# Performance work log

Measured on AMD Instinct MI355X. Metric: run time of the kernel, lower is better.

The kernel has to match this reference:

```python
import jax, jax.numpy as jnp
import numpy as np

D_MODEL = 1024
NUM_HEADS = 16
NEG_INF = jnp.float32(-(2.0 ** 32) + 1.0)  # matches TF's -2**32+1 padding value


def setup_inputs() -> dict:
    key = jax.random.key(0)
    ks = jax.random.split(key, 10)
    B, S, D = 4, 1024, D_MODEL
    s = 1.0 / np.sqrt(D)
    return {
        "q": jax.random.normal(ks[0], (B, S, D), jnp.float32),
        "k": jax.random.normal(ks[1], (B, S, D), jnp.float32),
        "v": jax.random.normal(ks[2], (B, S, D), jnp.float32),
        "mask": jax.random.randint(ks[3], (NUM_HEADS * B, 1, S), 0, 2, jnp.int32),
        "Wq": jax.random.normal(ks[4], (D, D), jnp.float32) * s,
        "bq": jnp.zeros((D,), jnp.float32),
        "Wk": jax.random.normal(ks[5], (D, D), jnp.float32) * s,
        "bk": jnp.zeros((D,), jnp.float32),
        "Wv": jax.random.normal(ks[6], (D, D), jnp.float32) * s,
        "bv": jnp.zeros((D,), jnp.float32),
    }


def _split_heads(x, h):
    # TF: concat(split(x, h, axis=2), axis=0) -> head index leading on batch dim
    B, S, D = x.shape
    dh = D // h
    return x.reshape(B, S, h, dh).transpose(2, 0, 1, 3).reshape(h * B, S, dh)


def _merge_heads(x, h):
    hB, S, dh = x.shape
    B = hB // h
    return x.reshape(h, B, S, dh).transpose(1, 2, 0, 3).reshape(B, S, h * dh)


def reference(q, k, v, mask, Wq, bq, Wk, bk, Wv, bv):
    h = NUM_HEADS
    qp = q @ Wq + bq
    kp = k @ Wk + bk
    vp = v @ Wv + bv
    qh = _split_heads(qp, h)  # [h*B, S, dh]
    kh = _split_heads(kp, h)
    vh = _split_heads(vp, h)
    dh = kh.shape[-1]
    logits = jnp.einsum('bqd,bkd->bqk', qh, kh) / jnp.sqrt(jnp.float32(dh))
    logits = jnp.where(mask == 0, NEG_INF, logits)  # padding mask, broadcast [h*B,1,S]
    S = qh.shape[1]
    causal = jnp.tril(jnp.ones((S, S), jnp.bool_))
    logits = jnp.where(causal[None], logits, NEG_INF)
    attn = jax.nn.softmax(logits, axis=-1)
    out = jnp.einsum('bqk,bkd->bqd', attn, vh)
    return _merge_heads(out, h)  # [B, S, d_model]
```

## Files before the change

### kernel.cpp

```cpp
#include <hip/hip_runtime.h>
#include <stdint.h>

#define DEV __device__ __forceinline__

typedef __attribute__((ext_vector_type(4))) float f32x4;
typedef __attribute__((ext_vector_type(8))) __bf16 bf16x8;
typedef __attribute__((ext_vector_type(8))) unsigned short ushort8;
typedef __attribute__((ext_vector_type(4))) unsigned short u16x4;
typedef __attribute__((ext_vector_type(4))) int i32x4;
typedef __attribute__((ext_vector_type(2))) unsigned int u32x2;

DEV unsigned short f2bf(float f) {
    union { float f; unsigned int u; } v; v.f = f;
    unsigned int r = v.u + 0x7FFFu + ((v.u >> 16) & 1u);
    return (unsigned short)(r >> 16);
}
DEV float bf2f(unsigned short u) {
    union { unsigned int u; float f; } v; v.u = ((unsigned int)u) << 16;
    return v.f;
}
DEV unsigned int cvt_pk_bf16(float lo, float hi) {
    unsigned int r;
    asm("v_cvt_pk_bf16_f32 %0, %1, %2" : "=v"(r) : "v"(lo), "v"(hi));
    return r;
}
DEV int swz(int o) { return o ^ ((o >> 3) & 0x70); }

DEV void gload_lds16(const void* gptr, void* lptr) {
    __builtin_amdgcn_global_load_lds(
        (const __attribute__((address_space(1))) unsigned int*)gptr,
        (__attribute__((address_space(3))) unsigned int*)lptr, 16, 0, 0);
}

__global__ void k_convert(const float* __restrict__ q, const float* __restrict__ k,
                          const float* __restrict__ v, unsigned short* __restrict__ qb,
                          unsigned short* __restrict__ kb, unsigned short* __restrict__ vb) {
    const int z = blockIdx.z;
    const float* src = z == 0 ? q : (z == 1 ? k : v);
    unsigned short* dst = z == 0 ? qb : (z == 1 ? kb : vb);
    const size_t idx = ((size_t)blockIdx.x * 256 + threadIdx.x) * 8;
    f32x4 a = *(const f32x4*)(src + idx);
    f32x4 b = *(const f32x4*)(src + idx + 4);
    ushort8 o;
    o[0] = f2bf(a[0]); o[1] = f2bf(a[1]); o[2] = f2bf(a[2]); o[3] = f2bf(a[3]);
    o[4] = f2bf(b[0]); o[5] = f2bf(b[1]); o[6] = f2bf(b[2]); o[7] = f2bf(b[3]);
    *(ushort8*)(dst + idx) = o;
}

__global__ void k_convw(const float* __restrict__ Wq, const float* __restrict__ Wk,
                        const float* __restrict__ Wv, unsigned short* __restrict__ wt) {
    __shared__ float tile[64 * 65];
    const int z = blockIdx.z;
    const float* W = z == 0 ? Wq : (z == 1 ? Wk : Wv);
    unsigned short* dst = wt + (size_t)z * 1048576;
    const int k0 = blockIdx.x * 64, n0 = blockIdx.y * 64;
    const int t = threadIdx.x;
#pragma unroll
    for (int i = 0; i < 4; i++) {
        const int idx = i * 256 + t;
        const int row = idx >> 4, c4 = (idx & 15) * 4;
        f32x4 val = *(const f32x4*)(W + (size_t)(k0 + row) * 1024 + n0 + c4);
#pragma unroll
        for (int j = 0; j < 4; j++) tile[row * 65 + c4 + j] = val[j];
    }
    __syncthreads();
#pragma unroll
    for (int i = 0; i < 2; i++) {
        const int idx = i * 256 + t;
        const int nrow = idx >> 3, c8 = (idx & 7) * 8;
        ushort8 o;
#pragma unroll
        for (int j = 0; j < 8; j++) o[j] = f2bf(tile[(c8 + j) * 65 + nrow]);
        *(ushort8*)(dst + (size_t)(n0 + nrow) * 1024 + k0 + c8) = o;
    }
}

__global__ __launch_bounds__(256) void k_proj(
    const unsigned short* __restrict__ qb, const unsigned short* __restrict__ kb,
    const unsigned short* __restrict__ vb, const unsigned short* __restrict__ wt,
    const float* __restrict__ bq, const float* __restrict__ bk, const float* __restrict__ bv,
    unsigned short* __restrict__ qh, unsigned short* __restrict__ kh,
    unsigned short* __restrict__ vt) {
    const int z = blockIdx.z;
    const unsigned short* A  = z == 0 ? qb : (z == 1 ? kb : vb);
    const unsigned short* Bt = wt + (size_t)z * 1048576;
    const float* bias = z == 0 ? bq : (z == 1 ? bk : bv);
    const float scale = z == 0 ? 0.18033688011112042f : 1.0f;

    __shared__ unsigned short sA[128 * 64];
    __shared__ unsigned short sB[128 * 64];

    const int tid = threadIdx.x;
    const int w = tid >> 6, lane = tid & 63;
    const int c = lane & 15, gq = lane >> 4;
    const int wrow = w >> 1, wcol = w & 1;
    const int m0 = blockIdx.y * 128, n0 = blockIdx.x * 128;
    const int lr = lane >> 3;
    const int lcs = ((lane & 7) ^ (lane >> 3)) * 8;

    f32x4 acc[4][4] = {};

    for (int kt = 0; kt < 16; kt++) {
        __syncthreads();
        const int kb0 = kt * 64;
#pragma unroll
        for (int i = 0; i < 4; i++) {
            const int rbase = w * 32 + i * 8;
            gload_lds16(A  + (size_t)(m0 + rbase + lr) * 1024 + kb0 + lcs,
                        (char*)sA + rbase * 128);
            gload_lds16(Bt + (size_t)(n0 + rbase + lr) * 1024 + kb0 + lcs,
                        (char*)sB + rbase * 128);
        }
        __syncthreads();
#pragma unroll
        for (int kk = 0; kk < 2; kk++) {
            bf16x8 af[4], bfr[4];
#pragma unroll
            for (int i = 0; i < 4; i++) {
                af[i]  = *(const bf16x8*)((char*)sA +
                          swz((wrow * 64 + i * 16 + c) * 128 + kk * 64 + gq * 16));
                bfr[i] = *(const bf16x8*)((char*)sB +
                          swz((wcol * 64 + i * 16 + c) * 128 + kk * 64 + gq * 16));
            }
#pragma unroll
            for (int mi = 0; mi < 4; mi++)
#pragma unroll
                for (int ni = 0; ni < 4; ni++)
                    acc[mi][ni] = __builtin_amdgcn_mfma_f32_16x16x32_bf16(
                        af[mi], bfr[ni], acc[mi][ni], 0, 0, 0);
        }
    }

    float bvals[4];
#pragma unroll
    for (int ni = 0; ni < 4; ni++) bvals[ni] = bias[n0 + wcol * 64 + ni * 16 + c];

    if (z < 2) {
        unsigned short* outp = z == 0 ? qh : kh;
#pragma unroll
        for (int mi = 0; mi < 4; mi++)
#pragma unroll
            for (int ni = 0; ni < 4; ni++) {
                const int n = n0 + wcol * 64 + ni * 16 + c;
                const int head = n >> 6, d = n & 63;
#pragma unroll
                for (int r = 0; r < 4; r++) {
                    const int m = m0 + wrow * 64 + mi * 16 + gq * 4 + r;
                    const int bb = m >> 10, s = m & 1023;
                    const float val = (acc[mi][ni][r] + bvals[ni]) * scale;
                    outp[(size_t)((head << 2) + bb) * 65536 + (size_t)s * 64 + d] = f2bf(val);
                }
            }
    } else {
#pragma unroll
        for (int mi = 0; mi < 4; mi++)
#pragma unroll
            for (int ni = 0; ni < 4; ni++) {
                const int n = n0 + wcol * 64 + ni * 16 + c;
                const int head = n >> 6, d = n & 63;
                const int mbase = m0 + wrow * 64 + mi * 16 + gq * 4;
                const int bb = mbase >> 10, sloc = mbase & 1023;
                u16x4 o;
#pragma unroll
                for (int r = 0; r < 4; r++) o[r] = f2bf(acc[mi][ni][r] + bvals[ni]);
                *(u16x4*)(vt + (size_t)((head << 2) + bb) * 65536 +
                          (size_t)d * 1024 + sloc) = o;
            }
    }
}

__global__ void k_vmean(const unsigned short* __restrict__ vt, float* __restrict__ vmean) {
    __shared__ float red[256];
    const int hb = blockIdx.x, t = threadIdx.x;
    const int d = t >> 2, part = t & 3;
    const unsigned short* p = vt + (size_t)hb * 65536 + (size_t)d * 1024 + part * 256;
    float sum = 0.f;
#pragma unroll 4
    for (int i = 0; i < 32; i++) {
        ushort8 v8 = *(const ushort8*)(p + i * 8);
#pragma unroll
        for (int j = 0; j < 8; j++) sum += bf2f(v8[j]);
    }
    red[t] = sum;
    __syncthreads();
    if (part == 0)
        vmean[hb * 64 + d] = (red[t] + red[t + 1] + red[t + 2] + red[t + 3]) * (1.0f / 1024.0f);
}

__global__ __launch_bounds__(256) void k_attn(
    const unsigned short* __restrict__ qh, const unsigned short* __restrict__ kh,
    const unsigned short* __restrict__ vt, const int* __restrict__ mask,
    const float* __restrict__ vmean, float* __restrict__ out,
    char* __restrict__ part) {
    __shared__ unsigned short sK[2][64 * 64];
    __shared__ unsigned short sV[2][64 * 64];
    __shared__ unsigned short sP[4 * 16 * 64];

    const int idx = blockIdx.x, hb = blockIdx.y;
    int qt, ch, nch;
    if (idx < 4)       { qt = idx;                 ch = 0;             nch = 1; }
    else if (idx < 12) { qt = 4 + ((idx - 4) >> 1);  ch = (idx - 4) & 1;  nch = 2; }
    else if (idx < 24) { int r = idx - 12; qt = 8 + r / 3; ch = r % 3;   nch = 3; }
    else               { qt = 12 + ((idx - 24) >> 2); ch = (idx - 24) & 3; nch = 4; }
    const int t0 = ch * 4;
    const int t1 = min(t0 + 4, qt + 1);

    const int tid = threadIdx.x;
    const int w = tid >> 6, lane = tid & 63;
    const int c = lane & 15, g = lane >> 4, g4 = g * 4;
    const int q0 = qt * 64 + w * 16;
    const int qg = q0 + c;
    const size_t hboff = (size_t)hb * 65536;
    const int* mp = mask + hb * 1024;
    unsigned short* pw = sP + w * 1024;

    bf16x8 aq[2];
#pragma unroll
    for (int kk = 0; kk < 2; kk++)
        aq[kk] = *(const bf16x8*)(qh + hboff + (size_t)qg * 64 + kk * 32 + g * 8);

    f32x4 oacc[4] = {};
    float lsum = 0.f, mrow = -1e30f;

    const int srow = tid >> 3, sch = tid & 7;
    const int ssc = (sch ^ (srow & 7)) * 8;

    auto stage = [&](int t, int buf) {
        const int kv0 = t * 64;
#pragma unroll
        for (int i = 0; i < 2; i++) {
            const int row = i * 32 + srow;
            gload_lds16(kh + hboff + (size_t)(kv0 + row) * 64 + ssc,
                        (char*)sK[buf] + row * 128 + sch * 16);
        }
#pragma unroll
        for (int i = 0; i < 2; i++) {
            const int row = i * 32 + srow;
            gload_lds16(vt + hboff + (size_t)row * 1024 + kv0 + ssc,
                        (char*)sV[buf] + row * 128 + sch * 16);
        }
    };

    stage(t0, 0);
    for (int t = t0; t < t1; t++) {
        const int cur = (t - t0) & 1;
        if (t + 1 < t1) {
            stage(t + 1, cur ^ 1);
            asm volatile("s_waitcnt vmcnt(4)" ::: "memory");
        } else {
            asm volatile("s_waitcnt vmcnt(0)" ::: "memory");
        }
        __builtin_amdgcn_s_barrier();
        __builtin_amdgcn_sched_barrier(0);

        const int kv0 = t * 64;
        const bool diag = (t == qt);
        const unsigned short* sKc = sK[cur];
        const unsigned short* sVc = sV[cur];

        f32x4 sacc[4] = {};
#pragma unroll
        for (int ns = 0; ns < 4; ns++)
#pragma unroll
            for (int kk = 0; kk < 2; kk++) {
                const bf16x8 bk = *(const bf16x8*)((char*)sKc +
                                    swz((ns * 16 + c) * 128 + kk * 64 + g * 16));
                sacc[ns] = __builtin_amdgcn_mfma_f32_16x16x32_bf16(bk, aq[kk], sacc[ns], 0, 0, 0);
            }

        float sv[4][4];
        float mx = -1e30f;
#pragma unroll
        for (int ns = 0; ns < 4; ns++) {
            const i32x4 mm = *(const i32x4*)(mp + kv0 + ns * 16 + g4);
#pragma unroll
            for (int r = 0; r < 4; r++) {
                float s = (mm[r] != 0) ? sacc[ns][r] : -1e30f;
                if (diag) s = (kv0 + ns * 16 + g4 + r <= qg) ? s : -1e30f;
                sv[ns][r] = s;
                mx = fmaxf(mx, s);
            }
        }
        mx = fmaxf(mx, __shfl_xor(mx, 16, 64));
        mx = fmaxf(mx, __shfl_xor(mx, 32, 64));
        const float mnew = fmaxf(mrow, mx);
        const float alpha = exp2f(mrow - mnew);
        mrow = mnew;

        float rs = 0.f;
        u32x2 pk[4];
#pragma unroll
        for (int ns = 0; ns < 4; ns++) {
            const float e0 = exp2f(sv[ns][0] - mnew);
            const float e1 = exp2f(sv[ns][1] - mnew);
            const float e2 = exp2f(sv[ns][2] - mnew);
            const float e3 = exp2f(sv[ns][3] - mnew);
            rs += (e0 + e1) + (e2 + e3);
            pk[ns][0] = cvt_pk_bf16(e0, e1);
            pk[ns][1] = cvt_pk_bf16(e2, e3);
        }
        rs += __shfl_xor(rs, 16, 64);
        rs += __shfl_xor(rs, 32, 64);
        lsum = lsum * alpha + rs;

#pragma unroll
        for (int ns = 0; ns < 4; ns++)
            *(u32x2*)((char*)pw + swz(c * 128 + (ns * 16 + g4) * 2)) = pk[ns];

        float av[4];
#pragma unroll
        for (int r = 0; r < 4; r++) av[r] = __shfl(alpha, g4 + r, 16);
#pragma unroll
        for (int nd = 0; nd < 4; nd++)
#pragma unroll
            for (int r = 0; r < 4; r++) oacc[nd][r] *= av[r];

        asm volatile("s_waitcnt lgkmcnt(0)" ::: "memory");
#pragma unroll
        for (int ks = 0; ks < 2; ks++) {
            const bf16x8 ap = *(const bf16x8*)((char*)pw + swz(c * 128 + ks * 64 + g * 16));
#pragma unroll
            for (int nd = 0; nd < 4; nd++) {
                const bf16x8 bvv = *(const bf16x8*)((char*)sVc +
                                     swz((nd * 16 + c) * 128 + ks * 64 + g * 16));
                oacc[nd] = __builtin_amdgcn_mfma_f32_16x16x32_bf16(ap, bvv, oacc[nd], 0, 0, 0);
            }
        }
        __builtin_amdgcn_sched_barrier(0);
        __builtin_amdgcn_s_barrier();
        __builtin_amdgcn_sched_barrier(0);
    }

    if (nch == 1) {
        const int bidx = hb & 3, head = hb >> 2;
        float lf[4], mf[4];
#pragma unroll
        for (int r = 0; r < 4; r++) {
            lf[r] = __shfl(lsum, g4 + r, 16);
            mf[r] = __shfl(mrow, g4 + r, 16);
        }
#pragma unroll
        for (int nd = 0; nd < 4; nd++)
#pragma unroll
            for (int r = 0; r < 4; r++) {
                const int s = q0 + g4 + r;
                const int dcol = nd * 16 + c;
                const float val = (mf[r] < -5e29f) ? vmean[hb * 64 + dcol]
                                                   : oacc[nd][r] / lf[r];
                out[(size_t)bidx * 1048576 + (size_t)s * 1024 + head * 64 + dcol] = val;
            }
    } else {
        char* sp = part + ((size_t)hb * 36 + (idx - 4)) * 8704;
        unsigned short* op = (unsigned short*)sp;
#pragma unroll
        for (int nd = 0; nd < 4; nd++)
#pragma unroll
            for (int r = 0; r < 4; r++)
                op[(w * 16 + g4 + r) * 64 + nd * 16 + c] = f2bf(oacc[nd][r]);
        if (g == 0) {
            float* mo = (float*)(sp + 8192);
            float* lo = (float*)(sp + 8448);
            mo[w * 16 + c] = mrow;
            lo[w * 16 + c] = lsum;
        }
    }
}

__global__ __launch_bounds__(256) void k_combine(
    const char* __restrict__ part, const float* __restrict__ vmean,
    float* __restrict__ out) {
    const int qt = 4 + blockIdx.x, hb = blockIdx.y;
    int nch, base;
    if (qt < 8)       { nch = 2; base = (qt - 4) * 2; }
    else if (qt < 12) { nch = 3; base = 8 + (qt - 8) * 3; }
    else              { nch = 4; base = 20 + (qt - 12) * 4; }
    const int t = threadIdx.x;
    const int row = t >> 2, d0 = (t & 3) * 16;
    const char* sp0 = part + ((size_t)hb * 36 + base) * 8704;

    float mi[4], li[4];
    float m = -1e30f;
#pragma unroll
    for (int i = 0; i < 4; i++)
        if (i < nch) {
            const char* sp = sp0 + (size_t)i * 8704;
            mi[i] = ((const float*)(sp + 8192))[row];
            li[i] = ((const float*)(sp + 8448))[row];
            m = fmaxf(m, mi[i]);
        }
    float L = 0.f;
    float o[16];
#pragma unroll
    for (int j = 0; j < 16; j++) o[j] = 0.f;
#pragma unroll
    for (int i = 0; i < 4; i++)
        if (i < nch) {
            const float wgt = exp2f(mi[i] - m);
            L += wgt * li[i];
            const unsigned short* op =
                (const unsigned short*)(sp0 + (size_t)i * 8704) + row * 64 + d0;
            ushort8 a = *(const ushort8*)op;
            ushort8 b = *(const ushort8*)(op + 8);
#pragma unroll
            for (int j = 0; j < 8; j++) {
                o[j]     += wgt * bf2f(a[j]);
                o[8 + j] += wgt * bf2f(b[j]);
            }
        }
    const int bidx = hb & 3, head = hb >> 2;
    float* dst = out + (size_t)bidx * 1048576 + (size_t)(qt * 64 + row) * 1024 + head * 64 + d0;
    if (m > -5e29f) {
        const float inv = 1.0f / L;
#pragma unroll
        for (int j = 0; j < 16; j++) dst[j] = o[j] * inv;
    } else {
#pragma unroll
        for (int j = 0; j < 16; j++) dst[j] = vmean[hb * 64 + d0 + j];
    }
}

extern "C" void kernel_launch(void* const* d_in, const int* in_sizes, int n_in,
                              void* d_out, int out_size, void* d_ws, size_t ws_size,
                              hipStream_t stream) {
    const float* q  = (const float*)d_in[0];
    const float* k  = (const float*)d_in[1];
    const float* v  = (const float*)d_in[2];
    const int* mask = (const int*)d_in[3];
    const float* Wq = (const float*)d_in[4];
    const float* bq = (const float*)d_in[5];
    const float* Wk = (const float*)d_in[6];
    const float* bk = (const float*)d_in[7];
    const float* Wv = (const float*)d_in[8];
    const float* bv = (const float*)d_in[9];
    float* out = (float*)d_out;

    unsigned short* qb = (unsigned short*)d_ws;
    unsigned short* kb = qb + 4194304;
    unsigned short* vb = kb + 4194304;
    unsigned short* wt = vb + 4194304;
    unsigned short* qh = wt + 3 * 1048576;
    unsigned short* kh = qh + 4194304;
    unsigned short* vh = kh + 4194304;
    unsigned short* vt = vh + 4194304;
    float* vmean = (float*)(vt + 4194304);
    char* part = (char*)qb;

    k_convert<<<dim3(2048, 1, 3), 256, 0, stream>>>(q, k, v, qb, kb, vb);
    k_convw<<<dim3(16, 16, 3), 256, 0, stream>>>(Wq, Wk, Wv, wt);
    k_proj<<<dim3(8, 32, 3), 256, 0, stream>>>(qb, kb, vb, wt, bq, bk, bv, qh, kh, vt);
    k_vmean<<<64, 256, 0, stream>>>(vt, vmean);
    k_attn<<<dim3(40, 64), 256, 0, stream>>>(qh, kh, vt, mask, vmean, out, part);
    k_combine<<<dim3(12, 64), 256, 0, stream>>>(part, vmean, out);
}
```

Measured before the change: 215.6 us.

## Double-buffer projection GEMM LDS loads, remap blocks, merge conversion kernels

Merges the activation and weight bf16 conversion kernels into one launch, which saves a kernel launch. The projection GEMM now double-buffers its A/B tiles in LDS so the next k-tile's global-to-LDS loads overlap the MFMA work on the current tile, with one barrier per iteration. Block indices are remapped so consecutive workgroups are spread across output tiles, which may change L2 locality. Doubling LDS to 64KB per block can reduce occupancy.

After: 211.4 us. About the same (-1.9%).

```diff
diff --git a/kernel.cpp b/kernel.cpp
--- a/kernel.cpp
+++ b/kernel.cpp
@@ -32,46 +32,48 @@
         (__attribute__((address_space(3))) unsigned int*)lptr, 16, 0, 0);
 }
 
-__global__ void k_convert(const float* __restrict__ q, const float* __restrict__ k,
-                          const float* __restrict__ v, unsigned short* __restrict__ qb,
-                          unsigned short* __restrict__ kb, unsigned short* __restrict__ vb) {
-    const int z = blockIdx.z;
-    const float* src = z == 0 ? q : (z == 1 ? k : v);
-    unsigned short* dst = z == 0 ? qb : (z == 1 ? kb : vb);
-    const size_t idx = ((size_t)blockIdx.x * 256 + threadIdx.x) * 8;
-    f32x4 a = *(const f32x4*)(src + idx);
-    f32x4 b = *(const f32x4*)(src + idx + 4);
-    ushort8 o;
-    o[0] = f2bf(a[0]); o[1] = f2bf(a[1]); o[2] = f2bf(a[2]); o[3] = f2bf(a[3]);
-    o[4] = f2bf(b[0]); o[5] = f2bf(b[1]); o[6] = f2bf(b[2]); o[7] = f2bf(b[3]);
-    *(ushort8*)(dst + idx) = o;
-}
-
-__global__ void k_convw(const float* __restrict__ Wq, const float* __restrict__ Wk,
-                        const float* __restrict__ Wv, unsigned short* __restrict__ wt) {
+__global__ void k_prep(const float* __restrict__ q, const float* __restrict__ k,
+                       const float* __restrict__ v, const float* __restrict__ Wq,
+                       const float* __restrict__ Wk, const float* __restrict__ Wv,
+                       unsigned short* __restrict__ qb, unsigned short* __restrict__ kb,
+                       unsigned short* __restrict__ vb, unsigned short* __restrict__ wt) {
     __shared__ float tile[64 * 65];
     const int z = blockIdx.z;
-    const float* W = z == 0 ? Wq : (z == 1 ? Wk : Wv);
-    unsigned short* dst = wt + (size_t)z * 1048576;
-    const int k0 = blockIdx.x * 64, n0 = blockIdx.y * 64;
+    const int bx = blockIdx.x;
     const int t = threadIdx.x;
-#pragma unroll
-    for (int i = 0; i < 4; i++) {
-        const int idx = i * 256 + t;
-        const int row = idx >> 4, c4 = (idx & 15) * 4;
-        f32x4 val = *(const f32x4*)(W + (size_t)(k0 + row) * 1024 + n0 + c4);
-#pragma unroll
-        for (int j = 0; j < 4; j++) tile[row * 65 + c4 + j] = val[j];
-    }
-    __syncthreads();
-#pragma unroll
-    for (int i = 0; i < 2; i++) {
-        const int idx = i * 256 + t;
-        const int nrow = idx >> 3, c8 = (idx & 7) * 8;
+    if (bx < 2048) {
+        const float* src = z == 0 ? q : (z == 1 ? k : v);
+        unsigned short* dst = z == 0 ? qb : (z == 1 ? kb : vb);
+        const size_t idx = ((size_t)bx * 256 + t) * 8;
+        f32x4 a = *(const f32x4*)(src + idx);
+        f32x4 b = *(const f32x4*)(src + idx + 4);
         ushort8 o;
-#pragma unroll
-        for (int j = 0; j < 8; j++) o[j] = f2bf(tile[(c8 + j) * 65 + nrow]);
-        *(ushort8*)(dst + (size_t)(n0 + nrow) * 1024 + k0 + c8) = o;
+        o[0] = f2bf(a[0]); o[1] = f2bf(a[1]); o[2] = f2bf(a[2]); o[3] = f2bf(a[3]);
+        o[4] = f2bf(b[0]); o[5] = f2bf(b[1]); o[6] = f2bf(b[2]); o[7] = f2bf(b[3]);
+        *(ushort8*)(dst + idx) = o;
+    } else {
+        const int b = bx - 2048;
+        const float* W = z == 0 ? Wq : (z == 1 ? Wk : Wv);
+        unsigned short* dst = wt + (size_t)z * 1048576;
+        const int k0 = (b & 15) * 64, n0 = (b >> 4) * 64;
+#pragma unroll
+        for (int i = 0; i < 4; i++) {
+            const int idx = i * 256 + t;
+            const int row = idx >> 4, c4 = (idx & 15) * 4;
+            f32x4 val = *(const f32x4*)(W + (size_t)(k0 + row) * 1024 + n0 + c4);
+#pragma unroll
+            for (int j = 0; j < 4; j++) tile[row * 65 + c4 + j] = val[j];
+        }
+        __syncthreads();
+#pragma unroll
+        for (int i = 0; i < 2; i++) {
+            const int idx = i * 256 + t;
+            const int nrow = idx >> 3, c8 = (idx & 7) * 8;
+            ushort8 o;
+#pragma unroll
+            for (int j = 0; j < 8; j++) o[j] = f2bf(tile[(c8 + j) * 65 + nrow]);
+            *(ushort8*)(dst + (size_t)(n0 + nrow) * 1024 + k0 + c8) = o;
+        }
     }
 }
 
@@ -87,39 +89,50 @@
     const float* bias = z == 0 ? bq : (z == 1 ? bk : bv);
     const float scale = z == 0 ? 0.18033688011112042f : 1.0f;
 
-    __shared__ unsigned short sA[128 * 64];
-    __shared__ unsigned short sB[128 * 64];
+    __shared__ unsigned short sA[2][128 * 64];
+    __shared__ unsigned short sB[2][128 * 64];
 
     const int tid = threadIdx.x;
     const int w = tid >> 6, lane = tid & 63;
     const int c = lane & 15, gq = lane >> 4;
     const int wrow = w >> 1, wcol = w & 1;
-    const int m0 = blockIdx.y * 128, n0 = blockIdx.x * 128;
+    const int orig = blockIdx.x;
+    const int wg = (orig & 7) * 32 + (orig >> 3);
+    const int n0 = (wg & 7) * 128;
+    const int m0 = (wg >> 3) * 128;
     const int lr = lane >> 3;
     const int lcs = ((lane & 7) ^ (lane >> 3)) * 8;
 
     f32x4 acc[4][4] = {};
 
-    for (int kt = 0; kt < 16; kt++) {
-        __syncthreads();
+    auto stageAB = [&](int kt, int buf) {
         const int kb0 = kt * 64;
 #pragma unroll
         for (int i = 0; i < 4; i++) {
             const int rbase = w * 32 + i * 8;
             gload_lds16(A  + (size_t)(m0 + rbase + lr) * 1024 + kb0 + lcs,
-                        (char*)sA + rbase * 128);
+                        (char*)sA[buf] + rbase * 128);
             gload_lds16(Bt + (size_t)(n0 + rbase + lr) * 1024 + kb0 + lcs,
-                        (char*)sB + rbase * 128);
-        }
-        __syncthreads();
+                        (char*)sB[buf] + rbase * 128);
+        }
+    };
+
+    stageAB(0, 0);
+    asm volatile("s_waitcnt vmcnt(0)" ::: "memory");
+    __builtin_amdgcn_s_barrier();
+
+    for (int kt = 0; kt < 16; kt++) {
+        const int cur = kt & 1;
+        if (kt < 15) stageAB(kt + 1, cur ^ 1);
+        __builtin_amdgcn_sched_barrier(0);
 #pragma unroll
         for (int kk = 0; kk < 2; kk++) {
             bf16x8 af[4], bfr[4];
 #pragma unroll
             for (int i = 0; i < 4; i++) {
-                af[i]  = *(const bf16x8*)((char*)sA +
+                af[i]  = *(const bf16x8*)((char*)sA[cur] +
                           swz((wrow * 64 + i * 16 + c) * 128 + kk * 64 + gq * 16));
-                bfr[i] = *(const bf16x8*)((char*)sB +
+                bfr[i] = *(const bf16x8*)((char*)sB[cur] +
                           swz((wcol * 64 + i * 16 + c) * 128 + kk * 64 + gq * 16));
             }
 #pragma unroll
@@ -129,6 +142,9 @@
                     acc[mi][ni] = __builtin_amdgcn_mfma_f32_16x16x32_bf16(
                         af[mi], bfr[ni], acc[mi][ni], 0, 0, 0);
         }
+        __builtin_amdgcn_sched_barrier(0);
+        asm volatile("s_waitcnt vmcnt(0)" ::: "memory");
+        __builtin_amdgcn_s_barrier();
     }
 
     float bvals[4];
@@ -445,9 +461,8 @@
     float* vmean = (float*)(vt + 4194304);
     char* part = (char*)qb;
 
-    k_convert<<<dim3(2048, 1, 3), 256, 0, stream>>>(q, k, v, qb, kb, vb);
-    k_convw<<<dim3(16, 16, 3), 256, 0, stream>>>(Wq, Wk, Wv, wt);
-    k_proj<<<dim3(8, 32, 3), 256, 0, stream>>>(qb, kb, vb, wt, bq, bk, bv, qh, kh, vt);
+    k_prep<<<dim3(2304, 1, 3), 256, 0, stream>>>(q, k, v, Wq, Wk, Wv, qb, kb, vb, wt);
+    k_proj<<<dim3(256, 1, 3), 256, 0, stream>>>(qb, kb, vb, wt, bq, bk, bv, qh, kh, vt);
     k_vmean<<<64, 256, 0, stream>>>(vt, vmean);
     k_attn<<<dim3(40, 64), 256, 0, stream>>>(qh, kh, vt, mask, vmean, out, part);
     k_combine<<<dim3(12, 64), 256, 0, stream>>>(part, vmean, out);
```
